# Kernel optimization log

Measured on AMD Instinct MI355X. Metric: run time of the kernel, lower is better.

## Reference

```python
import jax, jax.numpy as jnp
import numpy as np

WINDOW_SIZE = 11
CHANNEL = 3
SIGMA = 1.5
C1 = 0.01 ** 2
C2 = 0.03 ** 2


def _make_window():
    coords = jnp.arange(WINDOW_SIZE, dtype=jnp.float32) - WINDOW_SIZE // 2
    g = jnp.exp(-coords ** 2 / (2 * SIGMA ** 2))
    g = g / g.sum()
    w2d = jnp.outer(g, g)                      # (K, K)
    # (C, 1, K, K) depthwise kernel, OIHW with feature_group_count=C
    return jnp.broadcast_to(w2d[None, None], (CHANNEL, 1, WINDOW_SIZE, WINDOW_SIZE))


def _dwconv(x, w):
    # x: (1, C, H, W), w: (C, 1, K, K) -> same-padded depthwise conv
    pad = WINDOW_SIZE // 2
    return jax.lax.conv_general_dilated(
        x, w, window_strides=(1, 1), padding=[(pad, pad), (pad, pad)],
        feature_group_count=CHANNEL,
        dimension_numbers=('NCHW', 'OIHW', 'NCHW'))


def setup_inputs() -> dict:
    key = jax.random.key(0)
    k1, k2 = jax.random.split(key)
    H = W = 2048
    img1 = jax.random.uniform(k1, (H, W, 3), dtype=jnp.float32)
    img2 = jax.random.uniform(k2, (H, W, 3), dtype=jnp.float32)
    window = _make_window()
    return {"img1": img1, "img2": img2, "window": window}


def reference(img1, img2, window):
    # (H, W, C) -> (1, C, H, W)
    x = jnp.transpose(img1, (2, 0, 1))[None]
    y = jnp.transpose(img2, (2, 0, 1))[None]

    mu1 = _dwconv(x, window)
    mu2 = _dwconv(y, window)
    mu1_sq = mu1 ** 2
    mu2_sq = mu2 ** 2
    mu12 = mu1 * mu2

    sigma1_sq = _dwconv(x * x, window) - mu1_sq
    sigma2_sq = _dwconv(y * y, window) - mu2_sq
    sigma12 = _dwconv(x * y, window) - mu12

    ssim_map = ((2 * mu12 + C1) * (2 * sigma12 + C2)) / (
        (mu1_sq + mu2_sq + C1) * (sigma1_sq + sigma2_sq + C2))
    return 1.0 - ssim_map.mean()
```

## Files before the change

kernel.cpp:

```cpp
#include <hip/hip_runtime.h>
#include <math.h>

#define TILE 32
#define HALO 5
#define IH   42
#define LDSW 44
#define HBW  36

__global__ void zero_kernel(float* ws) { ws[0] = 0.0f; }

__global__ void finalize_kernel(const float* ws, float* out, float inv_n) {
    out[0] = 1.0f - ws[0] * inv_n;
}

__global__ __launch_bounds__(256, 3) void ssim_kernel(
    const float* __restrict__ img1, const float* __restrict__ img2,
    const float* __restrict__ window, float* __restrict__ accum,
    int H, int W)
{
    __shared__ float sx[IH][LDSW];
    __shared__ float sy[IH][LDSW];
    __shared__ float hb[5][IH][HBW];
    __shared__ float wsum[4];

    const int tid = threadIdx.x;
    const int x0  = blockIdx.x * TILE;
    const int y0  = blockIdx.y * TILE;

    float gr[11];
    {
        float inv = 1.0f / sqrtf(window[60]);
        #pragma unroll
        for (int t = 0; t < 11; ++t) gr[t] = window[55 + t] * inv;
    }

    float acc = 0.0f;

    for (int c = 0; c < 3; ++c) {
        __syncthreads();

        for (int item = tid; item < IH * 11; item += 256) {
            int r   = item / 11;
            int j4  = (item % 11) * 4;
            int gh  = y0 + r - HALO;
            int gx0 = x0 + j4 - HALO;
            bool rowok = ((unsigned)gh < (unsigned)H);
            float vx[4], vy[4];
            #pragma unroll
            for (int k = 0; k < 4; ++k) {
                int gx = gx0 + k;
                bool ok = rowok && ((unsigned)gx < (unsigned)W);
                long off = ((long)gh * W + gx) * 3 + c;
                vx[k] = ok ? img1[off] : 0.0f;
                vy[k] = ok ? img2[off] : 0.0f;
            }
            *(float4*)&sx[r][j4] = make_float4(vx[0], vx[1], vx[2], vx[3]);
            *(float4*)&sy[r][j4] = make_float4(vy[0], vy[1], vy[2], vy[3]);
        }
        __syncthreads();

        for (int item = tid; item < IH * 8; item += 256) {
            int r  = item >> 3;
            int j4 = (item & 7) * 4;
            float xv[16], yv[16];
            *(float4*)&xv[0]  = *(const float4*)&sx[r][j4];
            *(float4*)&xv[4]  = *(const float4*)&sx[r][j4 + 4];
            *(float4*)&xv[8]  = *(const float4*)&sx[r][j4 + 8];
            *(float4*)&xv[12] = *(const float4*)&sx[r][j4 + 12];
            *(float4*)&yv[0]  = *(const float4*)&sy[r][j4];
            *(float4*)&yv[4]  = *(const float4*)&sy[r][j4 + 4];
            *(float4*)&yv[8]  = *(const float4*)&sy[r][j4 + 8];
            *(float4*)&yv[12] = *(const float4*)&sy[r][j4 + 12];

            float xx[14], yy[14], xy[14];
            #pragma unroll
            for (int t = 0; t < 14; ++t) {
                xx[t] = xv[t] * xv[t];
                yy[t] = yv[t] * yv[t];
                xy[t] = xv[t] * yv[t];
            }
            float h0[4] = {0,0,0,0}, h1[4] = {0,0,0,0}, h2[4] = {0,0,0,0};
            float h3[4] = {0,0,0,0}, h4[4] = {0,0,0,0};
            #pragma unroll
            for (int jj = 0; jj < 4; ++jj) {
                #pragma unroll
                for (int t = 0; t < 11; ++t) {
                    float g = gr[t];
                    h0[jj] += g * xv[jj + t];
                    h1[jj] += g * yv[jj + t];
                    h2[jj] += g * xx[jj + t];
                    h3[jj] += g * yy[jj + t];
                    h4[jj] += g * xy[jj + t];
                }
            }
            *(float4*)&hb[0][r][j4] = make_float4(h0[0], h0[1], h0[2], h0[3]);
            *(float4*)&hb[1][r][j4] = make_float4(h1[0], h1[1], h1[2], h1[3]);
            *(float4*)&hb[2][r][j4] = make_float4(h2[0], h2[1], h2[2], h2[3]);
            *(float4*)&hb[3][r][j4] = make_float4(h3[0], h3[1], h3[2], h3[3]);
            *(float4*)&hb[4][r][j4] = make_float4(h4[0], h4[1], h4[2], h4[3]);
        }
        __syncthreads();

        {
            int j  = tid & 31;
            int i0 = (tid >> 5) * 4;
            float m1[4]  = {0,0,0,0}, m2[4]  = {0,0,0,0};
            float v11[4] = {0,0,0,0}, v22[4] = {0,0,0,0}, v12[4] = {0,0,0,0};
            #pragma unroll
            for (int t = 0; t < 14; ++t) {
                float b0 = hb[0][i0 + t][j];
                float b1 = hb[1][i0 + t][j];
                float b2 = hb[2][i0 + t][j];
                float b3 = hb[3][i0 + t][j];
                float b4 = hb[4][i0 + t][j];
                #pragma unroll
                for (int o = 0; o < 4; ++o) {
                    if (t - o >= 0 && t - o <= 10) {
                        float g = gr[t - o];
                        m1[o]  += g * b0;
                        m2[o]  += g * b1;
                        v11[o] += g * b2;
                        v22[o] += g * b3;
                        v12[o] += g * b4;
                    }
                }
            }
            const float C1 = 0.0001f, C2 = 0.0009f;
            #pragma unroll
            for (int o = 0; o < 4; ++o) {
                int gy = y0 + i0 + o, gx = x0 + j;
                if (gy < H && gx < W) {
                    float mu1 = m1[o], mu2 = m2[o];
                    float mu11 = mu1 * mu1, mu22 = mu2 * mu2, mu12 = mu1 * mu2;
                    float s11 = v11[o] - mu11;
                    float s22 = v22[o] - mu22;
                    float s12 = v12[o] - mu12;
                    float num = (2.0f * mu12 + C1) * (2.0f * s12 + C2);
                    float den = (mu11 + mu22 + C1) * (s11 + s22 + C2);
                    acc += num / den;
                }
            }
        }
    }

    #pragma unroll
    for (int off = 32; off > 0; off >>= 1)
        acc += __shfl_down(acc, off, 64);
    int lane = tid & 63, wid = tid >> 6;
    if (lane == 0) wsum[wid] = acc;
    __syncthreads();
    if (tid == 0)
        atomicAdd(accum, wsum[0] + wsum[1] + wsum[2] + wsum[3]);
}

extern "C" void kernel_launch(void* const* d_in, const int* in_sizes, int n_in,
                              void* d_out, int out_size, void* d_ws, size_t ws_size,
                              hipStream_t stream) {
    const float* img1   = (const float*)d_in[0];
    const float* img2   = (const float*)d_in[1];
    const float* window = (const float*)d_in[2];
    float* out = (float*)d_out;
    float* ws  = (float*)d_ws;

    long hw = (long)in_sizes[0] / 3;
    int W = (int)(sqrt((double)hw) + 0.5);
    int H = (int)(hw / W);

    float inv_n = (float)(1.0 / ((double)H * (double)W * 3.0));

    dim3 grid((W + TILE - 1) / TILE, (H + TILE - 1) / TILE);

    zero_kernel<<<1, 1, 0, stream>>>(ws);
    ssim_kernel<<<grid, 256, 0, stream>>>(img1, img2, window, ws, H, W);
    finalize_kernel<<<1, 1, 0, stream>>>(ws, out, inv_n);
}
```

Before: 215.9 us.

## Load raw pixels directly into registers, pack LDS planes, fuse finalize into last block

Drops the raw-pixel LDS staging stage: each thread now reads its 14-pixel strip straight from global memory into registers, with a branch-free fast path for interior tiles, and runs the horizontal pass on it. This removes one barrier and the sx/sy LDS buffers. The horizontal results are interleaved into float2-packed LDS planes so the vertical pass needs fewer LDS reads. The finalize kernel is replaced by a last-block-done atomic counter, and launch bounds go up to target 5 blocks per SM. The cost is redundant, strided global loads, since neighbouring threads overlap by 10 pixels each, plus higher register pressure.

```diff
diff --git a/kernel.cpp b/kernel.cpp
--- a/kernel.cpp
+++ b/kernel.cpp
@@ -4,23 +4,23 @@
 #define TILE 32
 #define HALO 5
 #define IH   42
-#define LDSW 44
-#define HBW  36
+#define HBW2 68
+#define HBW1 36
 
-__global__ void zero_kernel(float* ws) { ws[0] = 0.0f; }
-
-__global__ void finalize_kernel(const float* ws, float* out, float inv_n) {
-    out[0] = 1.0f - ws[0] * inv_n;
+__global__ void zero_kernel(float* ws) {
+    ws[0] = 0.0f;
+    ((unsigned*)ws)[1] = 0u;
 }
 
-__global__ __launch_bounds__(256, 3) void ssim_kernel(
+__global__ __launch_bounds__(256, 5) void ssim_kernel(
     const float* __restrict__ img1, const float* __restrict__ img2,
-    const float* __restrict__ window, float* __restrict__ accum,
-    int H, int W)
+    const float* __restrict__ window, float* __restrict__ ws,
+    float* __restrict__ out,
+    int H, int W, float inv_n, unsigned nblocks)
 {
-    __shared__ float sx[IH][LDSW];
-    __shared__ float sy[IH][LDSW];
-    __shared__ float hb[5][IH][HBW];
+    __shared__ float hb01[IH][HBW2];
+    __shared__ float hb23[IH][HBW2];
+    __shared__ float hb4 [IH][HBW1];
     __shared__ float wsum[4];
 
     const int tid = threadIdx.x;
@@ -34,70 +34,63 @@
         for (int t = 0; t < 11; ++t) gr[t] = window[55 + t] * inv;
     }
 
+    const bool interior = (x0 >= HALO) && (x0 + 37 <= W) &&
+                          (y0 >= HALO) && (y0 + 37 <= H);
+
     float acc = 0.0f;
 
     for (int c = 0; c < 3; ++c) {
         __syncthreads();
 
-        for (int item = tid; item < IH * 11; item += 256) {
-            int r   = item / 11;
-            int j4  = (item % 11) * 4;
-            int gh  = y0 + r - HALO;
+        for (int item = tid; item < IH * 8; item += 256) {
+            int r   = item >> 3;
+            int j4  = (item & 7) << 2;
+            int gh  = y0 + r  - HALO;
             int gx0 = x0 + j4 - HALO;
-            bool rowok = ((unsigned)gh < (unsigned)H);
-            float vx[4], vy[4];
-            #pragma unroll
-            for (int k = 0; k < 4; ++k) {
-                int gx = gx0 + k;
-                bool ok = rowok && ((unsigned)gx < (unsigned)W);
-                long off = ((long)gh * W + gx) * 3 + c;
-                vx[k] = ok ? img1[off] : 0.0f;
-                vy[k] = ok ? img2[off] : 0.0f;
+
+            float xv[14], yv[14];
+            if (interior) {
+                long base = ((long)gh * W + gx0) * 3 + c;
+                const float* p1 = img1 + base;
+                const float* p2 = img2 + base;
+                #pragma unroll
+                for (int k = 0; k < 14; ++k) {
+                    xv[k] = p1[k * 3];
+                    yv[k] = p2[k * 3];
+                }
+            } else {
+                bool rowok = ((unsigned)gh < (unsigned)H);
+                #pragma unroll
+                for (int k = 0; k < 14; ++k) {
+                    int gx = gx0 + k;
+                    bool ok = rowok && ((unsigned)gx < (unsigned)W);
+                    long off = ((long)gh * W + gx) * 3 + c;
+                    xv[k] = ok ? img1[off] : 0.0f;
+                    yv[k] = ok ? img2[off] : 0.0f;
+                }
             }
-            *(float4*)&sx[r][j4] = make_float4(vx[0], vx[1], vx[2], vx[3]);
-            *(float4*)&sy[r][j4] = make_float4(vy[0], vy[1], vy[2], vy[3]);
-        }
-        __syncthreads();
 
-        for (int item = tid; item < IH * 8; item += 256) {
-            int r  = item >> 3;
-            int j4 = (item & 7) * 4;
-            float xv[16], yv[16];
-            *(float4*)&xv[0]  = *(const float4*)&sx[r][j4];
-            *(float4*)&xv[4]  = *(const float4*)&sx[r][j4 + 4];
-            *(float4*)&xv[8]  = *(const float4*)&sx[r][j4 + 8];
-            *(float4*)&xv[12] = *(const float4*)&sx[r][j4 + 12];
-            *(float4*)&yv[0]  = *(const float4*)&sy[r][j4];
-            *(float4*)&yv[4]  = *(const float4*)&sy[r][j4 + 4];
-            *(float4*)&yv[8]  = *(const float4*)&sy[r][j4 + 8];
-            *(float4*)&yv[12] = *(const float4*)&sy[r][j4 + 12];
-
-            float xx[14], yy[14], xy[14];
-            #pragma unroll
-            for (int t = 0; t < 14; ++t) {
-                xx[t] = xv[t] * xv[t];
-                yy[t] = yv[t] * yv[t];
-                xy[t] = xv[t] * yv[t];
-            }
             float h0[4] = {0,0,0,0}, h1[4] = {0,0,0,0}, h2[4] = {0,0,0,0};
             float h3[4] = {0,0,0,0}, h4[4] = {0,0,0,0};
             #pragma unroll
-            for (int jj = 0; jj < 4; ++jj) {
+            for (int t = 0; t < 14; ++t) {
+                float a = xv[t], b = yv[t];
+                float aa = a * a, bb = b * b, ab = a * b;
                 #pragma unroll
-                for (int t = 0; t < 11; ++t) {
-                    float g = gr[t];
-                    h0[jj] += g * xv[jj + t];
-                    h1[jj] += g * yv[jj + t];
-                    h2[jj] += g * xx[jj + t];
-                    h3[jj] += g * yy[jj + t];
-                    h4[jj] += g * xy[jj + t];
+                for (int jj = 0; jj < 4; ++jj) {
+                    int k = t - jj;
+                    if (k >= 0 && k <= 10) {
+                        float g = gr[k];
+                        h0[jj] += g * a;  h1[jj] += g * b;
+                        h2[jj] += g * aa; h3[jj] += g * bb; h4[jj] += g * ab;
+                    }
                 }
             }
-            *(float4*)&hb[0][r][j4] = make_float4(h0[0], h0[1], h0[2], h0[3]);
-            *(float4*)&hb[1][r][j4] = make_float4(h1[0], h1[1], h1[2], h1[3]);
-            *(float4*)&hb[2][r][j4] = make_float4(h2[0], h2[1], h2[2], h2[3]);
-            *(float4*)&hb[3][r][j4] = make_float4(h3[0], h3[1], h3[2], h3[3]);
-            *(float4*)&hb[4][r][j4] = make_float4(h4[0], h4[1], h4[2], h4[3]);
+            *(float4*)&hb01[r][2*j4]     = make_float4(h0[0], h1[0], h0[1], h1[1]);
+            *(float4*)&hb01[r][2*j4 + 4] = make_float4(h0[2], h1[2], h0[3], h1[3]);
+            *(float4*)&hb23[r][2*j4]     = make_float4(h2[0], h3[0], h2[1], h3[1]);
+            *(float4*)&hb23[r][2*j4 + 4] = make_float4(h2[2], h3[2], h2[3], h3[3]);
+            *(float4*)&hb4 [r][j4]       = make_float4(h4[0], h4[1], h4[2], h4[3]);
         }
         __syncthreads();
 
@@ -108,20 +101,17 @@
             float v11[4] = {0,0,0,0}, v22[4] = {0,0,0,0}, v12[4] = {0,0,0,0};
             #pragma unroll
             for (int t = 0; t < 14; ++t) {
-                float b0 = hb[0][i0 + t][j];
-                float b1 = hb[1][i0 + t][j];
-                float b2 = hb[2][i0 + t][j];
-                float b3 = hb[3][i0 + t][j];
-                float b4 = hb[4][i0 + t][j];
+                float2 p01 = *(const float2*)&hb01[i0 + t][2 * j];
+                float2 p23 = *(const float2*)&hb23[i0 + t][2 * j];
+                float  p4  = hb4[i0 + t][j];
                 #pragma unroll
                 for (int o = 0; o < 4; ++o) {
-                    if (t - o >= 0 && t - o <= 10) {
-                        float g = gr[t - o];
-                        m1[o]  += g * b0;
-                        m2[o]  += g * b1;
-                        v11[o] += g * b2;
-                        v22[o] += g * b3;
-                        v12[o] += g * b4;
+                    int k = t - o;
+                    if (k >= 0 && k <= 10) {
+                        float g = gr[k];
+                        m1[o]  += g * p01.x;  m2[o]  += g * p01.y;
+                        v11[o] += g * p23.x;  v22[o] += g * p23.y;
+                        v12[o] += g * p4;
                     }
                 }
             }
@@ -149,8 +139,17 @@
     int lane = tid & 63, wid = tid >> 6;
     if (lane == 0) wsum[wid] = acc;
     __syncthreads();
-    if (tid == 0)
-        atomicAdd(accum, wsum[0] + wsum[1] + wsum[2] + wsum[3]);
+    if (tid == 0) {
+        float bsum = wsum[0] + wsum[1] + wsum[2] + wsum[3];
+        atomicAdd(ws, bsum);
+        __threadfence();
+        unsigned done = atomicAdd((unsigned*)ws + 1, 1u);
+        if (done == nblocks - 1) {
+            __threadfence();
+            float s = atomicAdd(ws, 0.0f);
+            out[0] = 1.0f - s * inv_n;
+        }
+    }
 }
 
 extern "C" void kernel_launch(void* const* d_in, const int* in_sizes, int n_in,
@@ -169,8 +168,9 @@
     float inv_n = (float)(1.0 / ((double)H * (double)W * 3.0));
 
     dim3 grid((W + TILE - 1) / TILE, (H + TILE - 1) / TILE);
+    unsigned nblocks = grid.x * grid.y;
 
     zero_kernel<<<1, 1, 0, stream>>>(ws);
-    ssim_kernel<<<grid, 256, 0, stream>>>(img1, img2, window, ws, H, W);
-    finalize_kernel<<<1, 1, 0, stream>>>(ws, out, inv_n);
+    ssim_kernel<<<grid, 256, 0, stream>>>(img1, img2, window, ws, out,
+                                          H, W, inv_n, nblocks);
 }
```

New measurement: 541.6 us. 151% more time.

## Prefetch next channel tile during vertical pass, fast interior loads, fuse finalize

Applied to the files above, without the earlier changes.

Moves the global-to-LDS load of the next channel so it runs after the horizontal pass, overlapping those loads with the vertical convolution and SSIM math. It also adds a branch-free load path for interior tiles that skips per-element bounds checks. The separate finalize kernel is folded into the main kernel through a last-block-done atomic counter, removing one launch. The reordering is safe because the sx/sy buffers are no longer read once the horizontal pass is done, but it adds register pressure and a serialized atomic tail.

```diff
diff --git a/kernel.cpp b/kernel.cpp
--- a/kernel.cpp
+++ b/kernel.cpp
@@ -7,16 +7,16 @@
 #define LDSW 44
 #define HBW  36
 
-__global__ void zero_kernel(float* ws) { ws[0] = 0.0f; }
-
-__global__ void finalize_kernel(const float* ws, float* out, float inv_n) {
-    out[0] = 1.0f - ws[0] * inv_n;
+__global__ void zero_kernel(float* ws) {
+    ws[0] = 0.0f;
+    ((unsigned*)ws)[1] = 0u;
 }
 
 __global__ __launch_bounds__(256, 3) void ssim_kernel(
     const float* __restrict__ img1, const float* __restrict__ img2,
-    const float* __restrict__ window, float* __restrict__ accum,
-    int H, int W)
+    const float* __restrict__ window, float* __restrict__ ws,
+    float* __restrict__ out,
+    int H, int W, float inv_n, unsigned nblocks)
 {
     __shared__ float sx[IH][LDSW];
     __shared__ float sy[IH][LDSW];
@@ -34,29 +34,46 @@
         for (int t = 0; t < 11; ++t) gr[t] = window[55 + t] * inv;
     }
 
-    float acc = 0.0f;
-
-    for (int c = 0; c < 3; ++c) {
-        __syncthreads();
-
+    const bool interior = (x0 >= HALO) && (x0 + 39 <= W) &&
+                          (y0 >= HALO) && (y0 + 37 <= H);
+
+    auto stage_a = [&](int c) {
         for (int item = tid; item < IH * 11; item += 256) {
             int r   = item / 11;
             int j4  = (item % 11) * 4;
             int gh  = y0 + r - HALO;
             int gx0 = x0 + j4 - HALO;
-            bool rowok = ((unsigned)gh < (unsigned)H);
             float vx[4], vy[4];
-            #pragma unroll
-            for (int k = 0; k < 4; ++k) {
-                int gx = gx0 + k;
-                bool ok = rowok && ((unsigned)gx < (unsigned)W);
-                long off = ((long)gh * W + gx) * 3 + c;
-                vx[k] = ok ? img1[off] : 0.0f;
-                vy[k] = ok ? img2[off] : 0.0f;
+            if (interior) {
+                long base = ((long)gh * W + gx0) * 3 + c;
+                const float* p1 = img1 + base;
+                const float* p2 = img2 + base;
+                #pragma unroll
+                for (int k = 0; k < 4; ++k) {
+                    vx[k] = p1[k * 3];
+                    vy[k] = p2[k * 3];
+                }
+            } else {
+                bool rowok = ((unsigned)gh < (unsigned)H);
+                #pragma unroll
+                for (int k = 0; k < 4; ++k) {
+                    int gx = gx0 + k;
+                    bool ok = rowok && ((unsigned)gx < (unsigned)W);
+                    long off = ((long)gh * W + gx) * 3 + c;
+                    vx[k] = ok ? img1[off] : 0.0f;
+                    vy[k] = ok ? img2[off] : 0.0f;
+                }
             }
             *(float4*)&sx[r][j4] = make_float4(vx[0], vx[1], vx[2], vx[3]);
             *(float4*)&sy[r][j4] = make_float4(vy[0], vy[1], vy[2], vy[3]);
         }
+    };
+
+    float acc = 0.0f;
+
+    stage_a(0);
+
+    for (int c = 0; c < 3; ++c) {
         __syncthreads();
 
         for (int item = tid; item < IH * 8; item += 256) {
@@ -101,6 +118,8 @@
         }
         __syncthreads();
 
+        if (c < 2) stage_a(c + 1);
+
         {
             int j  = tid & 31;
             int i0 = (tid >> 5) * 4;
@@ -149,8 +168,17 @@
     int lane = tid & 63, wid = tid >> 6;
     if (lane == 0) wsum[wid] = acc;
     __syncthreads();
-    if (tid == 0)
-        atomicAdd(accum, wsum[0] + wsum[1] + wsum[2] + wsum[3]);
+    if (tid == 0) {
+        float bsum = wsum[0] + wsum[1] + wsum[2] + wsum[3];
+        atomicAdd(ws, bsum);
+        __threadfence();
+        unsigned done = atomicAdd((unsigned*)ws + 1, 1u);
+        if (done == nblocks - 1) {
+            __threadfence();
+            float s = atomicAdd(ws, 0.0f);
+            out[0] = 1.0f - s * inv_n;
+        }
+    }
 }
 
 extern "C" void kernel_launch(void* const* d_in, const int* in_sizes, int n_in,
@@ -169,8 +197,9 @@
     float inv_n = (float)(1.0 / ((double)H * (double)W * 3.0));
 
     dim3 grid((W + TILE - 1) / TILE, (H + TILE - 1) / TILE);
+    unsigned nblocks = grid.x * grid.y;
 
     zero_kernel<<<1, 1, 0, stream>>>(ws);
-    ssim_kernel<<<grid, 256, 0, stream>>>(img1, img2, window, ws, H, W);
-    finalize_kernel<<<1, 1, 0, stream>>>(ws, out, inv_n);
+    ssim_kernel<<<grid, 256, 0, stream>>>(img1, img2, window, ws, out,
+                                          H, W, inv_n, nblocks);
 }
```

Result: slower. 293.8 us (+36.1%).
